# Kernel optimization log

Measured on AMD Instinct MI355X. Metric: run time of the kernel, lower is better.

## Reference

```python
import jax, jax.numpy as jnp
import numpy as np

B, T, E, V, A = 8192, 64, 128, 32000, 10


def setup_inputs() -> dict:
    key = jax.random.key(0)
    ks = jax.random.split(key, 8)
    return {
        "utterance": jax.random.randint(ks[0], (B, T), 0, V + 1, dtype=jnp.int64)
            if jax.config.jax_enable_x64 else jax.random.randint(ks[0], (B, T), 0, V + 1).astype(jnp.int32),
        "global_idxes": jnp.arange(B, dtype=jnp.int32),
        "emb_table": jax.random.normal(ks[1], (V + 1, E), jnp.float32) * 0.1,
        "w_ih": jax.random.normal(ks[2], (3 * E, E), jnp.float32) * 0.1,
        "w_hh": jax.random.normal(ks[3], (3 * E, E), jnp.float32) * 0.1,
        "b_ih": jax.random.normal(ks[4], (3 * E,), jnp.float32) * 0.1,
        "b_hh": jax.random.normal(ks[5], (3 * E,), jnp.float32) * 0.1,
        "w_out": jax.random.normal(ks[6], (A, E), jnp.float32) * 0.1,
        "b_out": jax.random.normal(ks[7], (A,), jnp.float32) * 0.1,
    }


def _gru_cell(x, h, w_ih, w_hh, b_ih, b_hh):
    # PyTorch GRUCell math
    gi = x @ w_ih.T + b_ih  # [B, 3E]
    gh = h @ w_hh.T + b_hh  # [B, 3E]
    i_r, i_z, i_n = jnp.split(gi, 3, axis=-1)
    h_r, h_z, h_n = jnp.split(gh, 3, axis=-1)
    r = jax.nn.sigmoid(i_r + h_r)
    z = jax.nn.sigmoid(i_z + h_z)
    n = jnp.tanh(i_n + r * h_n)
    return (1.0 - z) * n + z * h


def reference(utterance, global_idxes, emb_table, w_ih, w_hh, b_ih, b_hh, w_out, b_out):
    bsz = utterance.shape[0]
    h0 = jnp.zeros((bsz, emb_table.shape[1]), emb_table.dtype)
    alive0 = jnp.ones((bsz,), jnp.bool_)

    def step(carry, tok):
        h, out, alive = carry
        emb = emb_table[tok]                      # [B, E] gather
        h = _gru_cell(emb, h, w_ih, w_hh, b_ih, b_hh)
        # output_state only written for rows still alive entering this step
        out = jnp.where(alive[:, None], h, out)
        alive = alive & (tok != 0)                # mark_dead AFTER writing state
        return (h, out, alive), None

    tokens = utterance.T                          # [T, B]
    (_, out_state, _), _ = jax.lax.scan(step, (h0, h0, alive0), tokens)
    logits = out_state @ w_out.T + b_out          # [B, A]
    action_probs = jax.nn.softmax(logits, axis=-1)
    return action_probs
```

## Files before the change

kernel.cpp:

```cpp
#include <hip/hip_runtime.h>
#include <hip/hip_fp16.h>

#define Tt 64
#define Ee 128
#define Aa 10
#define Vv 32001

typedef __attribute__((ext_vector_type(8))) _Float16 half8;
typedef __attribute__((ext_vector_type(4))) _Float16 half4;
typedef __attribute__((ext_vector_type(4))) float f32x4;

#define L2E 1.44269504f

__device__ __forceinline__ float fast_rcp(float x) { return __builtin_amdgcn_rcpf(x); }
__device__ __forceinline__ float fast_exp2(float x) {
#if __has_builtin(__builtin_amdgcn_exp2f)
    return __builtin_amdgcn_exp2f(x);
#else
    return __expf(x * 0.69314718056f);
#endif
}

__device__ __forceinline__ half8 load_h8(const float* p) {
    f32x4 a = *(const f32x4*)p;
    f32x4 b = *(const f32x4*)(p + 4);
    half8 r;
    r[0] = (_Float16)a[0]; r[1] = (_Float16)a[1]; r[2] = (_Float16)a[2]; r[3] = (_Float16)a[3];
    r[4] = (_Float16)b[0]; r[5] = (_Float16)b[1]; r[6] = (_Float16)b[2]; r[7] = (_Float16)b[3];
    return r;
}
__device__ __forceinline__ half8 load_h8s(const float* p, float s) {
    f32x4 a = *(const f32x4*)p;
    f32x4 b = *(const f32x4*)(p + 4);
    half8 r;
#pragma unroll
    for (int j = 0; j < 4; ++j) { r[j] = (_Float16)(a[j] * s); r[4 + j] = (_Float16)(b[j] * s); }
    return r;
}

#define MFMA_F16(a, b, c)  __builtin_amdgcn_mfma_f32_16x16x32_f16(a, b, c, 0, 0, 0)

#define BAR_LGKM() do { \
    asm volatile("s_waitcnt lgkmcnt(0)" ::: "memory"); \
    __builtin_amdgcn_s_barrier(); \
} while (0)

__global__ __launch_bounds__(512, 2) void gi_precompute(
    const float* __restrict__ emb, const float* __restrict__ w_ih,
    const float* __restrict__ b_ih, const float* __restrict__ b_hh,
    char* __restrict__ gw) {
    __shared__ __align__(16) char xs[8192];
    const int tid = threadIdx.x;
    const int wv = tid >> 6;
    const int ln = tid & 63;
    const int fn = ln & 15;
    const int kg = ln >> 4;
    const int v0 = blockIdx.x * 32;
    const int gc = wv * 16 + fn;
    const int srow = tid >> 4;
    const int c8 = (tid & 15) << 3;

    {
        int v = v0 + srow; if (v >= Vv) v = Vv - 1;
        half8 hx = load_h8(emb + (size_t)v * Ee + c8);
        int off = (srow * 256 + c8 * 2) ^ ((srow & 7) << 4);
        *(half8*)(xs + off) = hx;
    }
    half8 wr[4], wz[4], wn[4];
#pragma unroll
    for (int kt = 0; kt < 4; ++kt) {
        int k0 = kt * 32 + kg * 8;
        wr[kt] = load_h8(w_ih + (size_t)gc * Ee + k0);
        wz[kt] = load_h8(w_ih + (size_t)(128 + gc) * Ee + k0);
        wn[kt] = load_h8(w_ih + (size_t)(256 + gc) * Ee + k0);
    }
    const float bcr = b_ih[gc] + b_hh[gc];
    const float bcz = b_ih[128 + gc] + b_hh[128 + gc];
    const float bcn = b_ih[256 + gc];
    __syncthreads();

    f32x4 ar[2], az[2], an[2];
#pragma unroll
    for (int mt = 0; mt < 2; ++mt) {
        ar[mt] = (f32x4){0.f, 0.f, 0.f, 0.f};
        az[mt] = (f32x4){0.f, 0.f, 0.f, 0.f};
        an[mt] = (f32x4){0.f, 0.f, 0.f, 0.f};
    }
#pragma unroll
    for (int kt = 0; kt < 4; ++kt)
#pragma unroll
        for (int mt = 0; mt < 2; ++mt) {
            int r = mt * 16 + fn;
            int off = (r * 256 + (kt * 32 + kg * 8) * 2) ^ ((r & 7) << 4);
            half8 ha = *(const half8*)(xs + off);
            ar[mt] = MFMA_F16(ha, wr[kt], ar[mt]);
            az[mt] = MFMA_F16(ha, wz[kt], az[mt]);
            an[mt] = MFMA_F16(ha, wn[kt], an[mt]);
        }
#pragma unroll
    for (int mt = 0; mt < 2; ++mt)
#pragma unroll
        for (int i = 0; i < 4; ++i) {
            int v = v0 + mt * 16 + kg * 4 + i;
            if (v < Vv) {
                half4 g;
                g[0] = (_Float16)((ar[mt][i] + bcr) * (-L2E));
                g[1] = (_Float16)((az[mt][i] + bcz) * (-L2E));
                g[2] = (_Float16)((an[mt][i] + bcn) * (2.f * L2E));
                g[3] = (_Float16)0.f;
                *(half4*)(gw + (size_t)v * 1024 + gc * 8) = g;
            }
        }
}

#define SM_BYTES 13120

__global__ __launch_bounds__(256, 2) void gru_quad_kernel(
    const int* __restrict__ utt, const char* __restrict__ gwc,
    const float* __restrict__ w_hh, const float* __restrict__ b_hh,
    const float* __restrict__ w_out, const float* __restrict__ b_out,
    float* __restrict__ out) {
    __shared__ __align__(16) char smem[SM_BYTES];
    int* tokb = (int*)smem;
    float* lg = (float*)(smem + 12288);
    int* tstar = (int*)(smem + 13056);
    float* outst = (float*)(smem + 4096);

    const int tid = threadIdx.x;
    const int wv = tid >> 6;
    const int ln = tid & 63;
    const int fn = ln & 15;
    const int kg = ln >> 4;
    const int row0 = blockIdx.x * 16;
    const int gc0 = wv * 32 + fn;
    const int gc1 = gc0 + 16;

    if (tid < 16) tstar[tid] = Tt - 1;
    *(f32x4*)(smem + 4096 + tid * 16) = (f32x4){0.f, 0.f, 0.f, 0.f};
    __syncthreads();
    {
        int4 tv = ((const int4*)(utt + (size_t)row0 * Tt))[tid];
        int4 sv = {tv.x << 10, tv.y << 10, tv.z << 10, tv.w << 10};
        ((int4*)tokb)[tid] = sv;
        int row = tid >> 4;
        int tq = (tid & 15) << 2;
        if (tv.x == 0) atomicMin(&tstar[row], tq);
        if (tv.y == 0) atomicMin(&tstar[row], tq + 1);
        if (tv.z == 0) atomicMin(&tstar[row], tq + 2);
        if (tv.w == 0) atomicMin(&tstar[row], tq + 3);
    }
    half8 whr[2][4], whz[2][4], whn[2][4];
#pragma unroll
    for (int kt = 0; kt < 4; ++kt) {
        int k0 = kt * 32 + kg * 8;
        whr[0][kt] = load_h8s(w_hh + (size_t)gc0 * Ee + k0, -L2E);
        whr[1][kt] = load_h8s(w_hh + (size_t)gc1 * Ee + k0, -L2E);
        whz[0][kt] = load_h8s(w_hh + (size_t)(128 + gc0) * Ee + k0, -L2E);
        whz[1][kt] = load_h8s(w_hh + (size_t)(128 + gc1) * Ee + k0, -L2E);
        whn[0][kt] = load_h8s(w_hh + (size_t)(256 + gc0) * Ee + k0, 2.f * L2E);
        whn[1][kt] = load_h8s(w_hh + (size_t)(256 + gc1) * Ee + k0, 2.f * L2E);
    }
    const float bhn2_0 = b_hh[256 + gc0] * (2.f * L2E);
    const float bhn2_1 = b_hh[256 + gc1] * (2.f * L2E);
    __syncthreads();

    int offk[4], wof[2][4];
#pragma unroll
    for (int kt = 0; kt < 4; ++kt)
        offk[kt] = (fn * 256 + (kt * 32 + kg * 8) * 2) ^ ((fn & 7) << 4);
#pragma unroll
    for (int i = 0; i < 4; ++i) {
        int row = kg * 4 + i;
        wof[0][i] = (row * 256 + gc0 * 2) ^ ((row & 7) << 4);
        wof[1][i] = (row * 256 + gc1 * 2) ^ ((row & 7) << 4);
    }

    int ts[4];
#pragma unroll
    for (int i = 0; i < 4; ++i) ts[i] = tstar[kg * 4 + i];

    half4 g0[4], g1[4];
#pragma unroll
    for (int i = 0; i < 4; ++i) {
        int to = tokb[(kg * 4 + i) * 64];
        g0[i] = *(const half4*)(gwc + to + gc0 * 8);
        g1[i] = *(const half4*)(gwc + to + gc1 * 8);
    }

    f32x4 h0 = (f32x4){0.f, 0.f, 0.f, 0.f}, o0 = h0;
    f32x4 h1 = h0, o1 = h0;

#pragma unroll 1
    for (int k = 0; k < Tt; ++k) {
        const char* hRd = smem + 4096 + (k & 1) * 4096;
        char* hWr = smem + 4096 + ((k + 1) & 1) * 4096;
        half8 f[4];
#pragma unroll
        for (int kt = 0; kt < 4; ++kt) f[kt] = *(const half8*)(hRd + offk[kt]);
        int t2 = (k < Tt - 1) ? k + 1 : Tt - 1;
        half4 gn0[4], gn1[4];
#pragma unroll
        for (int i = 0; i < 4; ++i) {
            int to = tokb[(kg * 4 + i) * 64 + t2];
            gn0[i] = *(const half4*)(gwc + to + gc0 * 8);
            gn1[i] = *(const half4*)(gwc + to + gc1 * 8);
        }
        f32x4 ar0, az0, an0, ar1, az1, an1;
#pragma unroll
        for (int i = 0; i < 4; ++i) {
            ar0[i] = (float)g0[i][0]; az0[i] = (float)g0[i][1]; an0[i] = bhn2_0;
            ar1[i] = (float)g1[i][0]; az1[i] = (float)g1[i][1]; an1[i] = bhn2_1;
        }
        __builtin_amdgcn_s_setprio(1);
#pragma unroll
        for (int kt = 0; kt < 4; ++kt) {
            ar0 = MFMA_F16(f[kt], whr[0][kt], ar0);
            az0 = MFMA_F16(f[kt], whz[0][kt], az0);
            an0 = MFMA_F16(f[kt], whn[0][kt], an0);
            ar1 = MFMA_F16(f[kt], whr[1][kt], ar1);
            az1 = MFMA_F16(f[kt], whz[1][kt], az1);
            an1 = MFMA_F16(f[kt], whn[1][kt], an1);
        }
        __builtin_amdgcn_s_setprio(0);
        bool wr = (k < Tt - 1);
#pragma unroll
        for (int i = 0; i < 4; ++i) {
            float ea = fast_exp2(ar0[i]);
            float eb = fast_exp2(az0[i]);
            float da = 1.f + ea, db = 1.f + eb;
            float R = fast_rcp(da * db);
            float rr = db * R, zz = da * R;
            float pnp = (float)g0[i][2] + rr * an0[i];
            float ec = fast_exp2(pnp);
            float nn = 1.f - 2.f * fast_rcp(ec + 1.f);
            float h = nn + zz * (h0[i] - nn);
            h0[i] = h;
            if (k == ts[i]) o0[i] = h;
            if (wr) *(_Float16*)(hWr + wof[0][i]) = (_Float16)h;
        }
#pragma unroll
        for (int i = 0; i < 4; ++i) {
            float ea = fast_exp2(ar1[i]);
            float eb = fast_exp2(az1[i]);
            float da = 1.f + ea, db = 1.f + eb;
            float R = fast_rcp(da * db);
            float rr = db * R, zz = da * R;
            float pnp = (float)g1[i][2] + rr * an1[i];
            float ec = fast_exp2(pnp);
            float nn = 1.f - 2.f * fast_rcp(ec + 1.f);
            float h = nn + zz * (h1[i] - nn);
            h1[i] = h;
            if (k == ts[i]) o1[i] = h;
            if (wr) *(_Float16*)(hWr + wof[1][i]) = (_Float16)h;
        }
#pragma unroll
        for (int i = 0; i < 4; ++i) { g0[i] = gn0[i]; g1[i] = gn1[i]; }
        BAR_LGKM();
    }

#pragma unroll
    for (int i = 0; i < 4; ++i) {
        outst[(kg * 4 + i) * Ee + gc0] = o0[i];
        outst[(kg * 4 + i) * Ee + gc1] = o1[i];
    }
    __syncthreads();

    if (tid < 16 * Aa) {
        int r = tid / Aa, a = tid % Aa;
        const float* wo = w_out + a * Ee;
        const float* os = outst + r * Ee;
        float s = b_out[a];
#pragma unroll
        for (int j = 0; j < Ee; j += 4) {
            f32x4 o = *(const f32x4*)(os + j);
            f32x4 w4 = *(const f32x4*)(wo + j);
            s += o[0] * w4[0] + o[1] * w4[1] + o[2] * w4[2] + o[3] * w4[3];
        }
        lg[r * 12 + a] = s;
    }
    __syncthreads();
    if (tid < 16) {
        float v[Aa];
        float mx = -1e30f;
#pragma unroll
        for (int a = 0; a < Aa; ++a) {
            v[a] = lg[tid * 12 + a];
            mx = fmaxf(mx, v[a]);
        }
        float sum = 0.f;
#pragma unroll
        for (int a = 0; a < Aa; ++a) {
            v[a] = __expf(v[a] - mx);
            sum += v[a];
        }
        float inv = fast_rcp(sum);
#pragma unroll
        for (int a = 0; a < Aa; ++a) out[(size_t)(row0 + tid) * Aa + a] = v[a] * inv;
    }
}

#define FSM_BYTES 21312
__global__ __launch_bounds__(512, 2) void gru_fallback_kernel(
    const int* __restrict__ utt, const float* __restrict__ emb,
    const float* __restrict__ w_ih, const float* __restrict__ w_hh,
    const float* __restrict__ b_ih, const float* __restrict__ b_hh,
    const float* __restrict__ w_out, const float* __restrict__ b_out,
    float* __restrict__ out) {
    __shared__ __align__(16) char smem[FSM_BYTES];
    int* tokb = (int*)smem;
    float* lg = (float*)(smem + 20480);
    int* tstar = (int*)(smem + 21248);
    float* outst = (float*)(smem + 4096);

    const int tid = threadIdx.x;
    const int wv = tid >> 6;
    const int ln = tid & 63;
    const int fn = ln & 15;
    const int kg = ln >> 4;
    const int row0 = blockIdx.x * 16;
    const int gc = wv * 16 + fn;
    const int srow = tid >> 5;
    const int c4 = (tid & 31) << 2;

    if (tid < 16) tstar[tid] = Tt - 1;
    *(float2*)(smem + 12288 + tid * 8) = (float2){0.f, 0.f};
    __syncthreads();
    {
        int2 tv = ((const int2*)(utt + (size_t)row0 * Tt))[tid];
        ((int2*)tokb)[tid] = tv;
        int row = tid >> 5;
        int tq = (tid & 31) << 1;
        if (tv.x == 0) atomicMin(&tstar[row], tq);
        if (tv.y == 0) atomicMin(&tstar[row], tq + 1);
    }
    half8 wir[4], wiz[4], win[4], whr[4], whz[4], whn[4];
#pragma unroll
    for (int kt = 0; kt < 4; ++kt) {
        int k0 = kt * 32 + kg * 8;
        wir[kt] = load_h8(w_ih + (size_t)gc * Ee + k0);
        wiz[kt] = load_h8(w_ih + (size_t)(128 + gc) * Ee + k0);
        win[kt] = load_h8(w_ih + (size_t)(256 + gc) * Ee + k0);
        whr[kt] = load_h8(w_hh + (size_t)gc * Ee + k0);
        whz[kt] = load_h8(w_hh + (size_t)(128 + gc) * Ee + k0);
        whn[kt] = load_h8(w_hh + (size_t)(256 + gc) * Ee + k0);
    }
    const float bcr = b_ih[gc] + b_hh[gc];
    const float bcz = b_ih[128 + gc] + b_hh[128 + gc];
    const float bin = b_ih[256 + gc];
    const float bhn = b_hh[256 + gc];
    __syncthreads();
    int ts[4];
#pragma unroll
    for (int i = 0; i < 4; ++i) ts[i] = tstar[kg * 4 + i];
    {
        int tok = tokb[srow * Tt];
        f32x4 a = *(const f32x4*)(emb + (size_t)tok * Ee + c4);
        half4 hx;
#pragma unroll
        for (int j = 0; j < 4; ++j) hx[j] = (_Float16)a[j];
        int off = (srow * 256 + c4 * 2) ^ ((srow & 7) << 4);
        *(half4*)(smem + 4096 + off) = hx;
    }
    __syncthreads();
    f32x4 hreg = (f32x4){0.f, 0.f, 0.f, 0.f};
    f32x4 oreg = (f32x4){0.f, 0.f, 0.f, 0.f};
    int cur = 0;
#pragma unroll 1
    for (int t = 0; t < Tt; ++t) {
        f32x4 pa;
        if (t < Tt - 1) {
            int tok = tokb[srow * Tt + t + 1];
            pa = *(const f32x4*)(emb + (size_t)tok * Ee + c4);
        }
        const char* xb = smem + 4096 + cur * 4096;
        const char* hb = smem + 12288 + cur * 4096;
        f32x4 ar = (f32x4){0.f, 0.f, 0.f, 0.f};
        f32x4 az = (f32x4){0.f, 0.f, 0.f, 0.f};
        f32x4 ain = (f32x4){0.f, 0.f, 0.f, 0.f};
        f32x4 ahn = (f32x4){0.f, 0.f, 0.f, 0.f};
        __builtin_amdgcn_s_setprio(1);
#pragma unroll
        for (int kt = 0; kt < 4; ++kt) {
            int off = (fn * 256 + (kt * 32 + kg * 8) * 2) ^ ((fn & 7) << 4);
            half8 xa = *(const half8*)(xb + off);
            half8 ha = *(const half8*)(hb + off);
            ar = MFMA_F16(xa, wir[kt], ar);
            ar = MFMA_F16(ha, whr[kt], ar);
            az = MFMA_F16(xa, wiz[kt], az);
            az = MFMA_F16(ha, whz[kt], az);
            ain = MFMA_F16(xa, win[kt], ain);
            ahn = MFMA_F16(ha, whn[kt], ahn);
        }
        __builtin_amdgcn_s_setprio(0);
        char* hn = smem + 12288 + (cur ^ 1) * 4096;
#pragma unroll
        for (int i = 0; i < 4; ++i) {
            float pr = ar[i] + bcr;
            float pz = az[i] + bcz;
            float rr = fast_rcp(1.f + __expf(-pr));
            float zz = fast_rcp(1.f + __expf(-pz));
            float pn = ain[i] + bin + rr * (ahn[i] + bhn);
            float e2 = __expf(2.f * pn);
            float nn = 1.f - 2.f * fast_rcp(e2 + 1.f);
            float h = (1.f - zz) * nn + zz * hreg[i];
            hreg[i] = h;
            if (t == ts[i]) oreg[i] = h;
            if (t < Tt - 1) {
                int row = kg * 4 + i;
                int off = (row * 256 + gc * 2) ^ ((row & 7) << 4);
                *(_Float16*)(hn + off) = (_Float16)h;
            }
        }
        if (t < Tt - 1) {
            half4 hx;
#pragma unroll
            for (int j = 0; j < 4; ++j) hx[j] = (_Float16)pa[j];
            int off = (srow * 256 + c4 * 2) ^ ((srow & 7) << 4);
            *(half4*)(smem + 4096 + (cur ^ 1) * 4096 + off) = hx;
        }
        __syncthreads();
        cur ^= 1;
    }
#pragma unroll
    for (int i = 0; i < 4; ++i) outst[(kg * 4 + i) * Ee + gc] = oreg[i];
    __syncthreads();
    if (tid < 16 * Aa) {
        int r = tid / Aa, a = tid % Aa;
        const float* wo = w_out + a * Ee;
        const float* os = outst + r * Ee;
        float s = b_out[a];
#pragma unroll
        for (int j = 0; j < Ee; j += 4) {
            f32x4 o = *(const f32x4*)(os + j);
            f32x4 w4 = *(const f32x4*)(wo + j);
            s += o[0] * w4[0] + o[1] * w4[1] + o[2] * w4[2] + o[3] * w4[3];
        }
        lg[r * 12 + a] = s;
    }
    __syncthreads();
    if (tid < 16) {
        float v[Aa];
        float mx = -1e30f;
#pragma unroll
        for (int a = 0; a < Aa; ++a) {
            v[a] = lg[tid * 12 + a];
            mx = fmaxf(mx, v[a]);
        }
        float sum = 0.f;
#pragma unroll
        for (int a = 0; a < Aa; ++a) {
            v[a] = __expf(v[a] - mx);
            sum += v[a];
        }
        float inv = fast_rcp(sum);
#pragma unroll
        for (int a = 0; a < Aa; ++a) out[(size_t)(row0 + tid) * Aa + a] = v[a] * inv;
    }
}

extern "C" void kernel_launch(void* const* d_in, const int* in_sizes, int n_in,
                              void* d_out, int out_size, void* d_ws, size_t ws_size,
                              hipStream_t stream) {
    (void)in_sizes; (void)n_in; (void)out_size;
    const int* utt = (const int*)d_in[0];
    const float* emb = (const float*)d_in[2];
    const float* wih = (const float*)d_in[3];
    const float* whh = (const float*)d_in[4];
    const float* bih = (const float*)d_in[5];
    const float* bhh = (const float*)d_in[6];
    const float* wout = (const float*)d_in[7];
    const float* bout = (const float*)d_in[8];
    const size_t need = (size_t)Vv * 1024;
    if (ws_size >= need) {
        char* gw = (char*)d_ws;
        gi_precompute<<<dim3((Vv + 31) / 32), 512, 0, stream>>>(emb, wih, bih, bhh, gw);
        gru_quad_kernel<<<512, 256, 0, stream>>>(utt, gw, whh, bhh, wout, bout, (float*)d_out);
    } else {
        gru_fallback_kernel<<<512, 512, 0, stream>>>(utt, emb, wih, whh, bih, bhh, wout, bout,
                                                     (float*)d_out);
    }
}
```

Baseline: 134.6 us.

## Split GRU hidden columns across eight waves and unroll timestep loop by two

Doubles the block from 4 to 8 waves so each wave owns 16 hidden columns instead of 32. This halves the per-wave MFMA chain and the gate math on the serial recurrence critical path. The time loop is manually unrolled by two, which removes the dynamic ping-pong buffer address computation and the gate-register copies between steps. In exchange, each barrier now synchronises twice as many waves, and with 512 blocks of 512 threads occupancy per CU may change.

```diff
diff --git a/kernel.cpp b/kernel.cpp
--- a/kernel.cpp
+++ b/kernel.cpp
@@ -115,7 +115,7 @@
 
 #define SM_BYTES 13120
 
-__global__ __launch_bounds__(256, 2) void gru_quad_kernel(
+__global__ __launch_bounds__(512, 2) void gru_octo_kernel(
     const int* __restrict__ utt, const char* __restrict__ gwc,
     const float* __restrict__ w_hh, const float* __restrict__ b_hh,
     const float* __restrict__ w_out, const float* __restrict__ b_out,
@@ -132,137 +132,107 @@
     const int fn = ln & 15;
     const int kg = ln >> 4;
     const int row0 = blockIdx.x * 16;
-    const int gc0 = wv * 32 + fn;
-    const int gc1 = gc0 + 16;
+    const int gc = wv * 16 + fn;
+    const int gc8 = gc * 8;
 
     if (tid < 16) tstar[tid] = Tt - 1;
-    *(f32x4*)(smem + 4096 + tid * 16) = (f32x4){0.f, 0.f, 0.f, 0.f};
+    *(float2*)(smem + 4096 + tid * 8) = (float2){0.f, 0.f};
     __syncthreads();
     {
-        int4 tv = ((const int4*)(utt + (size_t)row0 * Tt))[tid];
-        int4 sv = {tv.x << 10, tv.y << 10, tv.z << 10, tv.w << 10};
-        ((int4*)tokb)[tid] = sv;
-        int row = tid >> 4;
-        int tq = (tid & 15) << 2;
+        int2 tv = ((const int2*)(utt + (size_t)row0 * Tt))[tid];
+        int2 sv = {tv.x << 10, tv.y << 10};
+        ((int2*)tokb)[tid] = sv;
+        int row = tid >> 5;
+        int tq = (tid & 31) << 1;
         if (tv.x == 0) atomicMin(&tstar[row], tq);
         if (tv.y == 0) atomicMin(&tstar[row], tq + 1);
-        if (tv.z == 0) atomicMin(&tstar[row], tq + 2);
-        if (tv.w == 0) atomicMin(&tstar[row], tq + 3);
-    }
-    half8 whr[2][4], whz[2][4], whn[2][4];
+    }
+    half8 whr[4], whz[4], whn[4];
 #pragma unroll
     for (int kt = 0; kt < 4; ++kt) {
         int k0 = kt * 32 + kg * 8;
-        whr[0][kt] = load_h8s(w_hh + (size_t)gc0 * Ee + k0, -L2E);
-        whr[1][kt] = load_h8s(w_hh + (size_t)gc1 * Ee + k0, -L2E);
-        whz[0][kt] = load_h8s(w_hh + (size_t)(128 + gc0) * Ee + k0, -L2E);
-        whz[1][kt] = load_h8s(w_hh + (size_t)(128 + gc1) * Ee + k0, -L2E);
-        whn[0][kt] = load_h8s(w_hh + (size_t)(256 + gc0) * Ee + k0, 2.f * L2E);
-        whn[1][kt] = load_h8s(w_hh + (size_t)(256 + gc1) * Ee + k0, 2.f * L2E);
-    }
-    const float bhn2_0 = b_hh[256 + gc0] * (2.f * L2E);
-    const float bhn2_1 = b_hh[256 + gc1] * (2.f * L2E);
-    __syncthreads();
-
-    int offk[4], wof[2][4];
+        whr[kt] = load_h8s(w_hh + (size_t)gc * Ee + k0, -L2E);
+        whz[kt] = load_h8s(w_hh + (size_t)(128 + gc) * Ee + k0, -L2E);
+        whn[kt] = load_h8s(w_hh + (size_t)(256 + gc) * Ee + k0, 2.f * L2E);
+    }
+    const float bhn2 = b_hh[256 + gc] * (2.f * L2E);
+    __syncthreads();
+
+    int offk[4], wof[4], toff[4], ts[4];
 #pragma unroll
     for (int kt = 0; kt < 4; ++kt)
         offk[kt] = (fn * 256 + (kt * 32 + kg * 8) * 2) ^ ((fn & 7) << 4);
 #pragma unroll
     for (int i = 0; i < 4; ++i) {
         int row = kg * 4 + i;
-        wof[0][i] = (row * 256 + gc0 * 2) ^ ((row & 7) << 4);
-        wof[1][i] = (row * 256 + gc1 * 2) ^ ((row & 7) << 4);
-    }
-
-    int ts[4];
-#pragma unroll
-    for (int i = 0; i < 4; ++i) ts[i] = tstar[kg * 4 + i];
-
-    half4 g0[4], g1[4];
-#pragma unroll
-    for (int i = 0; i < 4; ++i) {
-        int to = tokb[(kg * 4 + i) * 64];
-        g0[i] = *(const half4*)(gwc + to + gc0 * 8);
-        g1[i] = *(const half4*)(gwc + to + gc1 * 8);
-    }
-
-    f32x4 h0 = (f32x4){0.f, 0.f, 0.f, 0.f}, o0 = h0;
-    f32x4 h1 = h0, o1 = h0;
+        wof[i] = (row * 256 + gc * 2) ^ ((row & 7) << 4);
+        toff[i] = row * 64;
+        ts[i] = tstar[row];
+    }
+
+    half4 gA[4], gB[4];
+#pragma unroll
+    for (int i = 0; i < 4; ++i)
+        gA[i] = *(const half4*)(gwc + tokb[toff[i]] + gc8);
+
+    f32x4 h = (f32x4){0.f, 0.f, 0.f, 0.f};
+    f32x4 o = h;
+
+#define STEP(K, RD, WR, GCUR, GNXT) do {                                      \
+        half8 f0 = *(const half8*)((RD) + offk[0]);                           \
+        half8 f1 = *(const half8*)((RD) + offk[1]);                           \
+        half8 f2 = *(const half8*)((RD) + offk[2]);                           \
+        half8 f3 = *(const half8*)((RD) + offk[3]);                           \
+        int t2 = (K) + 1; if (t2 > Tt - 1) t2 = Tt - 1;                       \
+        GNXT[0] = *(const half4*)(gwc + tokb[toff[0] + t2] + gc8);            \
+        GNXT[1] = *(const half4*)(gwc + tokb[toff[1] + t2] + gc8);            \
+        GNXT[2] = *(const half4*)(gwc + tokb[toff[2] + t2] + gc8);            \
+        GNXT[3] = *(const half4*)(gwc + tokb[toff[3] + t2] + gc8);            \
+        f32x4 ar, az, an;                                                     \
+        _Pragma("unroll")                                                     \
+        for (int i = 0; i < 4; ++i) {                                         \
+            ar[i] = (float)GCUR[i][0]; az[i] = (float)GCUR[i][1];             \
+            an[i] = bhn2;                                                     \
+        }                                                                     \
+        __builtin_amdgcn_s_setprio(1);                                        \
+        ar = MFMA_F16(f0, whr[0], ar); az = MFMA_F16(f0, whz[0], az);         \
+        an = MFMA_F16(f0, whn[0], an);                                        \
+        ar = MFMA_F16(f1, whr[1], ar); az = MFMA_F16(f1, whz[1], az);         \
+        an = MFMA_F16(f1, whn[1], an);                                        \
+        ar = MFMA_F16(f2, whr[2], ar); az = MFMA_F16(f2, whz[2], az);         \
+        an = MFMA_F16(f2, whn[2], an);                                        \
+        ar = MFMA_F16(f3, whr[3], ar); az = MFMA_F16(f3, whz[3], az);         \
+        an = MFMA_F16(f3, whn[3], an);                                        \
+        __builtin_amdgcn_s_setprio(0);                                        \
+        bool wr_ = (K) < Tt - 1;                                              \
+        _Pragma("unroll")                                                     \
+        for (int i = 0; i < 4; ++i) {                                         \
+            float ea = fast_exp2(ar[i]);                                      \
+            float eb = fast_exp2(az[i]);                                      \
+            float da = 1.f + ea, db = 1.f + eb;                               \
+            float R = fast_rcp(da * db);                                      \
+            float rr = db * R, zz = da * R;                                   \
+            float pnp = (float)GCUR[i][2] + rr * an[i];                       \
+            float ec = fast_exp2(pnp);                                        \
+            float nn = 1.f - 2.f * fast_rcp(ec + 1.f);                        \
+            float hv = nn + zz * (h[i] - nn);                                 \
+            h[i] = hv;                                                        \
+            if ((K) == ts[i]) o[i] = hv;                                      \
+            if (wr_) *(_Float16*)((WR) + wof[i]) = (_Float16)hv;              \
+        }                                                                     \
+    } while (0)
 
 #pragma unroll 1
-    for (int k = 0; k < Tt; ++k) {
-        const char* hRd = smem + 4096 + (k & 1) * 4096;
-        char* hWr = smem + 4096 + ((k + 1) & 1) * 4096;
-        half8 f[4];
-#pragma unroll
-        for (int kt = 0; kt < 4; ++kt) f[kt] = *(const half8*)(hRd + offk[kt]);
-        int t2 = (k < Tt - 1) ? k + 1 : Tt - 1;
-        half4 gn0[4], gn1[4];
-#pragma unroll
-        for (int i = 0; i < 4; ++i) {
-            int to = tokb[(kg * 4 + i) * 64 + t2];
-            gn0[i] = *(const half4*)(gwc + to + gc0 * 8);
-            gn1[i] = *(const half4*)(gwc + to + gc1 * 8);
-        }
-        f32x4 ar0, az0, an0, ar1, az1, an1;
-#pragma unroll
-        for (int i = 0; i < 4; ++i) {
-            ar0[i] = (float)g0[i][0]; az0[i] = (float)g0[i][1]; an0[i] = bhn2_0;
-            ar1[i] = (float)g1[i][0]; az1[i] = (float)g1[i][1]; an1[i] = bhn2_1;
-        }
-        __builtin_amdgcn_s_setprio(1);
-#pragma unroll
-        for (int kt = 0; kt < 4; ++kt) {
-            ar0 = MFMA_F16(f[kt], whr[0][kt], ar0);
-            az0 = MFMA_F16(f[kt], whz[0][kt], az0);
-            an0 = MFMA_F16(f[kt], whn[0][kt], an0);
-            ar1 = MFMA_F16(f[kt], whr[1][kt], ar1);
-            az1 = MFMA_F16(f[kt], whz[1][kt], az1);
-            an1 = MFMA_F16(f[kt], whn[1][kt], an1);
-        }
-        __builtin_amdgcn_s_setprio(0);
-        bool wr = (k < Tt - 1);
-#pragma unroll
-        for (int i = 0; i < 4; ++i) {
-            float ea = fast_exp2(ar0[i]);
-            float eb = fast_exp2(az0[i]);
-            float da = 1.f + ea, db = 1.f + eb;
-            float R = fast_rcp(da * db);
-            float rr = db * R, zz = da * R;
-            float pnp = (float)g0[i][2] + rr * an0[i];
-            float ec = fast_exp2(pnp);
-            float nn = 1.f - 2.f * fast_rcp(ec + 1.f);
-            float h = nn + zz * (h0[i] - nn);
-            h0[i] = h;
-            if (k == ts[i]) o0[i] = h;
-            if (wr) *(_Float16*)(hWr + wof[0][i]) = (_Float16)h;
-        }
-#pragma unroll
-        for (int i = 0; i < 4; ++i) {
-            float ea = fast_exp2(ar1[i]);
-            float eb = fast_exp2(az1[i]);
-            float da = 1.f + ea, db = 1.f + eb;
-            float R = fast_rcp(da * db);
-            float rr = db * R, zz = da * R;
-            float pnp = (float)g1[i][2] + rr * an1[i];
-            float ec = fast_exp2(pnp);
-            float nn = 1.f - 2.f * fast_rcp(ec + 1.f);
-            float h = nn + zz * (h1[i] - nn);
-            h1[i] = h;
-            if (k == ts[i]) o1[i] = h;
-            if (wr) *(_Float16*)(hWr + wof[1][i]) = (_Float16)h;
-        }
-#pragma unroll
-        for (int i = 0; i < 4; ++i) { g0[i] = gn0[i]; g1[i] = gn1[i]; }
+    for (int k = 0; k < Tt; k += 2) {
+        STEP(k, smem + 4096, smem + 8192, gA, gB);
         BAR_LGKM();
-    }
-
-#pragma unroll
-    for (int i = 0; i < 4; ++i) {
-        outst[(kg * 4 + i) * Ee + gc0] = o0[i];
-        outst[(kg * 4 + i) * Ee + gc1] = o1[i];
-    }
+        STEP(k + 1, smem + 8192, smem + 4096, gB, gA);
+        BAR_LGKM();
+    }
+#undef STEP
+
+#pragma unroll
+    for (int i = 0; i < 4; ++i) outst[(kg * 4 + i) * Ee + gc] = o[i];
     __syncthreads();
 
     if (tid < 16 * Aa) {
@@ -272,9 +242,9 @@
         float s = b_out[a];
 #pragma unroll
         for (int j = 0; j < Ee; j += 4) {
-            f32x4 o = *(const f32x4*)(os + j);
+            f32x4 ov = *(const f32x4*)(os + j);
             f32x4 w4 = *(const f32x4*)(wo + j);
-            s += o[0] * w4[0] + o[1] * w4[1] + o[2] * w4[2] + o[3] * w4[3];
+            s += ov[0] * w4[0] + ov[1] * w4[1] + ov[2] * w4[2] + ov[3] * w4[3];
         }
         lg[r * 12 + a] = s;
     }
@@ -474,7 +444,7 @@
     if (ws_size >= need) {
         char* gw = (char*)d_ws;
         gi_precompute<<<dim3((Vv + 31) / 32), 512, 0, stream>>>(emb, wih, bih, bhh, gw);
-        gru_quad_kernel<<<512, 256, 0, stream>>>(utt, gw, whh, bhh, wout, bout, (float*)d_out);
+        gru_octo_kernel<<<512, 512, 0, stream>>>(utt, gw, whh, bhh, wout, bout, (float*)d_out);
     } else {
         gru_fallback_kernel<<<512, 512, 0, stream>>>(utt, emb, wih, whh, bih, bhh, wout, bout,
                                                      (float*)d_out);
```

New measurement: 153.1 us. +13.7%, slower.
